# Kernel optimization log

Hardware: AMD Instinct MI355X
Metric: run time of the kernel (lower is better)

## Reference

```python
import jax, jax.numpy as jnp
import numpy as np

S = 32  # spatial_size
EPS = 1e-8

def _adaptive_avg_pool(x, s):
    b, c, h, w = x.shape
    kh, kw = h // s, w // s
    return x.reshape(b, c, s, kh, s, kw).mean(axis=(3, 5))

def _gram_cosine(x):
    # x: [B, C, s, s] -> rows: [B*s*s, C]
    b, c, s, _ = x.shape
    rows = x.reshape(b, c, s * s).transpose(0, 2, 1).reshape(b * s * s, c)
    norms = jnp.sqrt(jnp.sum(rows * rows, axis=-1, keepdims=True))
    xn = rows / jnp.maximum(norms, EPS)
    return xn @ xn.T  # [N, N]

def setup_inputs() -> dict:
    key = jax.random.key(0)
    k1, k2 = jax.random.split(key)
    p1 = jax.random.normal(k1, (8, 64, 128, 128), dtype=jnp.float32)
    p2 = jax.random.normal(k2, (8, 64, 128, 128), dtype=jnp.float32)
    return {"p1": p1, "p2": p2}

def reference(p1, p2):
    sim_a = _gram_cosine(_adaptive_avg_pool(p1, S))
    sim_b = _gram_cosine(_adaptive_avg_pool(p2, S))
    return jnp.mean((sim_a - sim_b) ** 2)
```

## Files before the change

kernel.cpp:

```cpp
#include <hip/hip_runtime.h>

typedef float f4 __attribute__((ext_vector_type(4)));
typedef float f2 __attribute__((ext_vector_type(2)));

#define PAD 68
#define NPART 256
#define PART_STRIDE 12288


__device__ __forceinline__ void lds_barrier() {
    asm volatile("s_waitcnt lgkmcnt(0)" ::: "memory");
    __builtin_amdgcn_s_barrier();
    __builtin_amdgcn_sched_barrier(0);
}

__global__ __launch_bounds__(1024) void fused_gram_kernel(
    const float* __restrict__ p1, const float* __restrict__ p2,
    float* __restrict__ partials, unsigned* __restrict__ cnt)
{
    __shared__ float la[2][8 * PAD];
    __shared__ float lb[2][8 * PAD];
    const int t  = threadIdx.x;
    const int b  = blockIdx.x >> 5;
    const int oi = blockIdx.x & 31;

    if (blockIdx.x == 0 && t == 0) *cnt = 0u;

    const int m   = t >> 9;
    const int c   = (t >> 3) & 63;
    const int oj8 = t & 7;
    const float* src = m ? p2 : p1;
    const long base = (long)((b * 64 + c) * 128 + oi * 4) * 128 + oj8 * 4;
    float* dst0 = m ? lb[0] : la[0];
    float* dst1 = m ? lb[1] : la[1];

    const int l  = t & 63;
    const int w  = t >> 6;
    const int nm = w >> 3, nr = w & 7;

    const int c1 = (t >> 5) * 2;
    const int c2 = (t & 31) * 2;
    f2 aa0 = {}, aa1 = {}, ab0 = {}, ab1 = {}, bb0 = {}, bb1 = {};

    auto issue = [&](int q, f4& R0, f4& R1, f4& R2, f4& R3) {
        const float* s = src + base + q * 32;
        R0 = *(const f4*)(s);
        R1 = *(const f4*)(s + 128);
        R2 = *(const f4*)(s + 256);
        R3 = *(const f4*)(s + 384);
    };
    auto pool = [&](const f4& R0, const f4& R1, const f4& R2, const f4& R3,
                    float* dst) {
        const f4 v = (R0 + R1) + (R2 + R3);
        dst[oj8 * PAD + c] = ((v[0] + v[1]) + (v[2] + v[3])) * 0.0625f;
    };
    auto normphase = [&](int bi) {
        float* rowp = (nm ? lb[bi] : la[bi]) + nr * PAD;
        const float v = rowp[l];
        float ss = v * v;
        ss += __shfl_xor(ss, 1);
        ss += __shfl_xor(ss, 2);
        ss += __shfl_xor(ss, 4);
        ss += __shfl_xor(ss, 8);
        ss += __shfl_xor(ss, 16);
        ss += __shfl_xor(ss, 32);
        rowp[l] = v * (1.0f / fmaxf(sqrtf(ss), 1e-8f));
    };
    auto gram = [&](int bi) {
        #pragma unroll
        for (int r = 0; r < 8; ++r) {
            const f2 a1 = *(const f2*)&la[bi][r * PAD + c1];
            const f2 a2 = *(const f2*)&la[bi][r * PAD + c2];
            const f2 b1 = *(const f2*)&lb[bi][r * PAD + c1];
            const f2 b2 = *(const f2*)&lb[bi][r * PAD + c2];
            aa0 += a2 * a1[0];  aa1 += a2 * a1[1];
            ab0 += b2 * a1[0];  ab1 += b2 * a1[1];
            bb0 += b2 * b1[0];  bb1 += b2 * b1[1];
        }
    };

    f4 A0, A1, A2, A3, B0, B1, B2, B3;
    issue(0, A0, A1, A2, A3);
    issue(1, B0, B1, B2, B3);

    pool(A0, A1, A2, A3, dst0);  lds_barrier();
    normphase(0);                lds_barrier();
    issue(2, A0, A1, A2, A3);
    gram(0);

    pool(B0, B1, B2, B3, dst1);  lds_barrier();
    normphase(1);                lds_barrier();
    issue(3, B0, B1, B2, B3);
    gram(1);

    pool(A0, A1, A2, A3, dst0);  lds_barrier();
    normphase(0);                lds_barrier();
    gram(0);

    pool(B0, B1, B2, B3, dst1);  lds_barrier();
    normphase(1);                lds_barrier();
    gram(1);

    float* P = partials + (long)blockIdx.x * PART_STRIDE;
    *(f2*)&P[0 * 4096 + (c1    ) * 64 + c2] = aa0;
    *(f2*)&P[0 * 4096 + (c1 + 1) * 64 + c2] = aa1;
    *(f2*)&P[1 * 4096 + (c1    ) * 64 + c2] = ab0;
    *(f2*)&P[1 * 4096 + (c1 + 1) * 64 + c2] = ab1;
    *(f2*)&P[2 * 4096 + (c1    ) * 64 + c2] = bb0;
    *(f2*)&P[2 * 4096 + (c1 + 1) * 64 + c2] = bb1;
}

__global__ __launch_bounds__(256) void reduce_kernel(
    const float* __restrict__ partials, float* __restrict__ bpart,
    unsigned* __restrict__ cnt, float* __restrict__ out)
{
    __shared__ float red[3][16][17];
    __shared__ float vred[16];
    __shared__ float fr[256];
    __shared__ unsigned last_flag;
    const int t  = threadIdx.x;
    const int el = t & 15;
    const int pc = t >> 4;
    const int e  = blockIdx.x * 16 + el;

    float saa = 0.f, sab = 0.f, sbb = 0.f;
    #pragma unroll 4
    for (int i = 0; i < 16; ++i) {
        const float* P = partials + (long)(pc * 16 + i) * PART_STRIDE;
        saa += P[e];
        sab += P[4096 + e];
        sbb += P[8192 + e];
    }
    red[0][el][pc] = saa; red[1][el][pc] = sab; red[2][el][pc] = sbb;
    __syncthreads();

    if (t < 16) {
        float a = 0.f, mm = 0.f, bv = 0.f;
        #pragma unroll
        for (int p = 0; p < 16; ++p) {
            a  += red[0][t][p];
            mm += red[1][t][p];
            bv += red[2][t][p];
        }
        vred[t] = fmaf(a, a, fmaf(bv, bv, -2.0f * (mm * mm)));
    }
    __syncthreads();

    if (t == 0) {
        float s = 0.f;
        #pragma unroll
        for (int i = 0; i < 16; ++i) s += vred[i];
        __hip_atomic_store(&bpart[blockIdx.x], s, __ATOMIC_RELEASE,
                           __HIP_MEMORY_SCOPE_AGENT);
        unsigned old = __hip_atomic_fetch_add(cnt, 1u, __ATOMIC_ACQ_REL,
                                              __HIP_MEMORY_SCOPE_AGENT);
        last_flag = (old == NPART - 1) ? 1u : 0u;
    }
    __syncthreads();

    if (last_flag) {
        fr[t] = __hip_atomic_load(&bpart[t], __ATOMIC_ACQUIRE,
                                  __HIP_MEMORY_SCOPE_AGENT);
        __syncthreads();
        for (int s2 = 128; s2 > 0; s2 >>= 1) {
            if (t < s2) fr[t] += fr[t + s2];
            __syncthreads();
        }
        if (t == 0) out[0] = fr[0] * (1.0f / 67108864.0f);
    }
}

extern "C" void kernel_launch(void* const* d_in, const int* in_sizes, int n_in,
                              void* d_out, int out_size, void* d_ws, size_t ws_size,
                              hipStream_t stream)
{
    const float* p1 = (const float*)d_in[0];
    const float* p2 = (const float*)d_in[1];
    float* ws       = (float*)d_ws;
    float* partials = ws;
    float* bpart    = ws + (long)NPART * PART_STRIDE;
    unsigned* cnt   = (unsigned*)(ws + 3146240);

    fused_gram_kernel<<<NPART, 1024, 0, stream>>>(p1, p2, partials, cnt);
    reduce_kernel   <<<NPART, 256, 0, stream>>>(partials, bpart, cnt, (float*)d_out);
}
```

Measured before the change: 33.67 us.

## Fuse final reduction into gram kernel via global atomics and last-block reduce

Removes the separate reduce kernel and the 256 per-block partial Gram buffers. Each block now atomically adds its 64x64x3 partial Gram values into one shared 12288-float accumulator. The last block to finish, found with an atomic counter, computes the squared-difference sum and writes the output. A memset is added to zero the accumulator and counter, and the input loads switch to nontemporal. The trade is about 12 MB of partial writes and reads plus one kernel launch against roughly 3M contended float atomics to L2 and an extra memset launch.

```diff
diff --git a/kernel.cpp b/kernel.cpp
--- a/kernel.cpp
+++ b/kernel.cpp
@@ -4,8 +4,7 @@
 typedef float f2 __attribute__((ext_vector_type(2)));
 
 #define PAD 68
-#define NPART 256
-#define PART_STRIDE 12288
+#define NBLK 256
 
 
 __device__ __forceinline__ void lds_barrier() {
@@ -14,17 +13,17 @@
     __builtin_amdgcn_sched_barrier(0);
 }
 
-__global__ __launch_bounds__(1024) void fused_gram_kernel(
+__global__ __launch_bounds__(1024) void fused_all_kernel(
     const float* __restrict__ p1, const float* __restrict__ p2,
-    float* __restrict__ partials, unsigned* __restrict__ cnt)
+    float* __restrict__ gram, unsigned* __restrict__ cnt,
+    float* __restrict__ out)
 {
     __shared__ float la[2][8 * PAD];
     __shared__ float lb[2][8 * PAD];
+    __shared__ unsigned lastf;
     const int t  = threadIdx.x;
     const int b  = blockIdx.x >> 5;
     const int oi = blockIdx.x & 31;
-
-    if (blockIdx.x == 0 && t == 0) *cnt = 0u;
 
     const int m   = t >> 9;
     const int c   = (t >> 3) & 63;
@@ -44,10 +43,10 @@
 
     auto issue = [&](int q, f4& R0, f4& R1, f4& R2, f4& R3) {
         const float* s = src + base + q * 32;
-        R0 = *(const f4*)(s);
-        R1 = *(const f4*)(s + 128);
-        R2 = *(const f4*)(s + 256);
-        R3 = *(const f4*)(s + 384);
+        R0 = __builtin_nontemporal_load((const f4*)(s));
+        R1 = __builtin_nontemporal_load((const f4*)(s + 128));
+        R2 = __builtin_nontemporal_load((const f4*)(s + 256));
+        R3 = __builtin_nontemporal_load((const f4*)(s + 384));
     };
     auto pool = [&](const f4& R0, const f4& R1, const f4& R2, const f4& R3,
                     float* dst) {
@@ -66,7 +65,7 @@
         ss += __shfl_xor(ss, 32);
         rowp[l] = v * (1.0f / fmaxf(sqrtf(ss), 1e-8f));
     };
-    auto gram = [&](int bi) {
+    auto gramacc = [&](int bi) {
         #pragma unroll
         for (int r = 0; r < 8; ++r) {
             const f2 a1 = *(const f2*)&la[bi][r * PAD + c1];
@@ -86,83 +85,58 @@
     pool(A0, A1, A2, A3, dst0);  lds_barrier();
     normphase(0);                lds_barrier();
     issue(2, A0, A1, A2, A3);
-    gram(0);
+    gramacc(0);
 
     pool(B0, B1, B2, B3, dst1);  lds_barrier();
     normphase(1);                lds_barrier();
     issue(3, B0, B1, B2, B3);
-    gram(1);
+    gramacc(1);
 
     pool(A0, A1, A2, A3, dst0);  lds_barrier();
     normphase(0);                lds_barrier();
-    gram(0);
+    gramacc(0);
 
     pool(B0, B1, B2, B3, dst1);  lds_barrier();
     normphase(1);                lds_barrier();
-    gram(1);
+    gramacc(1);
 
-    float* P = partials + (long)blockIdx.x * PART_STRIDE;
-    *(f2*)&P[0 * 4096 + (c1    ) * 64 + c2] = aa0;
-    *(f2*)&P[0 * 4096 + (c1 + 1) * 64 + c2] = aa1;
-    *(f2*)&P[1 * 4096 + (c1    ) * 64 + c2] = ab0;
-    *(f2*)&P[1 * 4096 + (c1 + 1) * 64 + c2] = ab1;
-    *(f2*)&P[2 * 4096 + (c1    ) * 64 + c2] = bb0;
-    *(f2*)&P[2 * 4096 + (c1 + 1) * 64 + c2] = bb1;
-}
+    {
+        float* G0 = gram +           c1 * 64 + c2;
+        float* G1 = gram + 4096 +    c1 * 64 + c2;
+        float* G2 = gram + 8192 +    c1 * 64 + c2;
+        atomicAdd(G0,      aa0[0]); atomicAdd(G0 + 1,  aa0[1]);
+        atomicAdd(G0 + 64, aa1[0]); atomicAdd(G0 + 65, aa1[1]);
+        atomicAdd(G1,      ab0[0]); atomicAdd(G1 + 1,  ab0[1]);
+        atomicAdd(G1 + 64, ab1[0]); atomicAdd(G1 + 65, ab1[1]);
+        atomicAdd(G2,      bb0[0]); atomicAdd(G2 + 1,  bb0[1]);
+        atomicAdd(G2 + 64, bb1[0]); atomicAdd(G2 + 65, bb1[1]);
+    }
 
-__global__ __launch_bounds__(256) void reduce_kernel(
-    const float* __restrict__ partials, float* __restrict__ bpart,
-    unsigned* __restrict__ cnt, float* __restrict__ out)
-{
-    __shared__ float red[3][16][17];
-    __shared__ float vred[16];
-    __shared__ float fr[256];
-    __shared__ unsigned last_flag;
-    const int t  = threadIdx.x;
-    const int el = t & 15;
-    const int pc = t >> 4;
-    const int e  = blockIdx.x * 16 + el;
-
-    float saa = 0.f, sab = 0.f, sbb = 0.f;
-    #pragma unroll 4
-    for (int i = 0; i < 16; ++i) {
-        const float* P = partials + (long)(pc * 16 + i) * PART_STRIDE;
-        saa += P[e];
-        sab += P[4096 + e];
-        sbb += P[8192 + e];
-    }
-    red[0][el][pc] = saa; red[1][el][pc] = sab; red[2][el][pc] = sbb;
     __syncthreads();
-
-    if (t < 16) {
-        float a = 0.f, mm = 0.f, bv = 0.f;
-        #pragma unroll
-        for (int p = 0; p < 16; ++p) {
-            a  += red[0][t][p];
-            mm += red[1][t][p];
-            bv += red[2][t][p];
-        }
-        vred[t] = fmaf(a, a, fmaf(bv, bv, -2.0f * (mm * mm)));
+    if (t == 0) {
+        unsigned old = __hip_atomic_fetch_add(cnt, 1u, __ATOMIC_ACQ_REL,
+                                              __HIP_MEMORY_SCOPE_AGENT);
+        lastf = (old == NBLK - 1) ? 1u : 0u;
     }
     __syncthreads();
 
-    if (t == 0) {
-        float s = 0.f;
+    if (lastf) {
+        float vsum = 0.f;
         #pragma unroll
-        for (int i = 0; i < 16; ++i) s += vred[i];
-        __hip_atomic_store(&bpart[blockIdx.x], s, __ATOMIC_RELEASE,
-                           __HIP_MEMORY_SCOPE_AGENT);
-        unsigned old = __hip_atomic_fetch_add(cnt, 1u, __ATOMIC_ACQ_REL,
-                                              __HIP_MEMORY_SCOPE_AGENT);
-        last_flag = (old == NPART - 1) ? 1u : 0u;
-    }
-    __syncthreads();
-
-    if (last_flag) {
-        fr[t] = __hip_atomic_load(&bpart[t], __ATOMIC_ACQUIRE,
-                                  __HIP_MEMORY_SCOPE_AGENT);
+        for (int i = 0; i < 4; ++i) {
+            const int e = t * 4 + i;
+            const float a  = __hip_atomic_load(&gram[e],
+                                __ATOMIC_RELAXED, __HIP_MEMORY_SCOPE_AGENT);
+            const float mm = __hip_atomic_load(&gram[4096 + e],
+                                __ATOMIC_RELAXED, __HIP_MEMORY_SCOPE_AGENT);
+            const float bb = __hip_atomic_load(&gram[8192 + e],
+                                __ATOMIC_RELAXED, __HIP_MEMORY_SCOPE_AGENT);
+            vsum += fmaf(a, a, fmaf(bb, bb, -2.0f * (mm * mm)));
+        }
+        float* fr = (float*)la;
+        fr[t] = vsum;
         __syncthreads();
-        for (int s2 = 128; s2 > 0; s2 >>= 1) {
+        for (int s2 = 512; s2 > 0; s2 >>= 1) {
             if (t < s2) fr[t] += fr[t + s2];
             __syncthreads();
         }
@@ -176,11 +150,11 @@
 {
     const float* p1 = (const float*)d_in[0];
     const float* p2 = (const float*)d_in[1];
-    float* ws       = (float*)d_ws;
-    float* partials = ws;
-    float* bpart    = ws + (long)NPART * PART_STRIDE;
-    unsigned* cnt   = (unsigned*)(ws + 3146240);
+    float* ws   = (float*)d_ws;
+    float* gram = ws;
+    unsigned* cnt = (unsigned*)(ws + 12288);
 
-    fused_gram_kernel<<<NPART, 1024, 0, stream>>>(p1, p2, partials, cnt);
-    reduce_kernel   <<<NPART, 256, 0, stream>>>(partials, bpart, cnt, (float*)d_out);
+    hipMemsetAsync(ws, 0, (12288 + 1) * sizeof(float), stream);
+    fused_all_kernel<<<NBLK, 1024, 0, stream>>>(p1, p2, gram, cnt,
+                                                (float*)d_out);
 }
```

Result: slower. 70.46 us (+109.3%).

## Warp-specialize gram kernel into producer/consumer waves with LDS flag sync

Applied to the files above, without the earlier changes.

Splits the 1024-thread block into 8 producer waves that load and pool the input tiles, and 8 consumer waves that normalize and accumulate the gram products. Block-wide barriers are replaced by LDS atomic counters (ready/normd/done) with spin-waits, so loading the next tile can overlap with gram computation. Consumers now compute 2x4 output tiles with f4 loads and stores instead of 2x2. The cost is spin-wait polling, each consumer thread holding twice the accumulators, and half as many threads doing each phase's arithmetic.

```diff
diff --git a/kernel.cpp b/kernel.cpp
--- a/kernel.cpp
+++ b/kernel.cpp
@@ -8,9 +8,8 @@
 #define PART_STRIDE 12288
 
 
-__device__ __forceinline__ void lds_barrier() {
+__device__ __forceinline__ void lds_fence() {
     asm volatile("s_waitcnt lgkmcnt(0)" ::: "memory");
-    __builtin_amdgcn_s_barrier();
     __builtin_amdgcn_sched_barrier(0);
 }
 
@@ -20,94 +19,131 @@
 {
     __shared__ float la[2][8 * PAD];
     __shared__ float lb[2][8 * PAD];
+    __shared__ unsigned ready[2];
+    __shared__ unsigned normd[2];
+    __shared__ unsigned done[2];
     const int t  = threadIdx.x;
     const int b  = blockIdx.x >> 5;
     const int oi = blockIdx.x & 31;
 
     if (blockIdx.x == 0 && t == 0) *cnt = 0u;
-
-    const int m   = t >> 9;
-    const int c   = (t >> 3) & 63;
-    const int oj8 = t & 7;
-    const float* src = m ? p2 : p1;
-    const long base = (long)((b * 64 + c) * 128 + oi * 4) * 128 + oj8 * 4;
-    float* dst0 = m ? lb[0] : la[0];
-    float* dst1 = m ? lb[1] : la[1];
-
-    const int l  = t & 63;
-    const int w  = t >> 6;
-    const int nm = w >> 3, nr = w & 7;
-
-    const int c1 = (t >> 5) * 2;
-    const int c2 = (t & 31) * 2;
-    f2 aa0 = {}, aa1 = {}, ab0 = {}, ab1 = {}, bb0 = {}, bb1 = {};
-
-    auto issue = [&](int q, f4& R0, f4& R1, f4& R2, f4& R3) {
-        const float* s = src + base + q * 32;
-        R0 = *(const f4*)(s);
-        R1 = *(const f4*)(s + 128);
-        R2 = *(const f4*)(s + 256);
-        R3 = *(const f4*)(s + 384);
+    if (t < 2) { ready[t] = 0u; normd[t] = 0u; done[t] = 0u; }
+    asm volatile("s_waitcnt lgkmcnt(0)" ::: "memory");
+    __builtin_amdgcn_s_barrier();
+    __builtin_amdgcn_sched_barrier(0);
+
+    const int wave = t >> 6;
+    const int lane = t & 63;
+
+    if (wave < 8) {
+        const int pt  = t;
+        const int m   = pt >> 8;
+        const int pm  = pt & 255;
+        const int cl  = pm >> 3;
+        const int oj8 = pm & 7;
+        const float* src = m ? p2 : p1;
+        const long base0 = (long)((b * 64 + cl     ) * 128 + oi * 4) * 128 + oj8 * 4;
+        const long base1 = (long)((b * 64 + cl + 32) * 128 + oi * 4) * 128 + oj8 * 4;
+        float* dst[2] = { (m ? lb[0] : la[0]), (m ? lb[1] : la[1]) };
+
+        f4 X[8], Y[8];
+        auto issue = [&](int q, f4* R) {
+            const float* s0 = src + base0 + q * 32;
+            const float* s1 = src + base1 + q * 32;
+            R[0] = *(const f4*)(s0);       R[1] = *(const f4*)(s0 + 128);
+            R[2] = *(const f4*)(s0 + 256); R[3] = *(const f4*)(s0 + 384);
+            R[4] = *(const f4*)(s1);       R[5] = *(const f4*)(s1 + 128);
+            R[6] = *(const f4*)(s1 + 256); R[7] = *(const f4*)(s1 + 384);
+        };
+        auto pool = [&](const f4* R, int buf) {
+            const f4 v0 = (R[0] + R[1]) + (R[2] + R[3]);
+            const f4 v1 = (R[4] + R[5]) + (R[6] + R[7]);
+            dst[buf][oj8 * PAD + cl]      = ((v0[0]+v0[1])+(v0[2]+v0[3])) * 0.0625f;
+            dst[buf][oj8 * PAD + cl + 32] = ((v1[0]+v1[1])+(v1[2]+v1[3])) * 0.0625f;
+        };
+        auto mark = [&](int buf) {
+            lds_fence();
+            if (lane == 0)
+                __hip_atomic_fetch_add(&ready[buf], 1u, __ATOMIC_RELAXED,
+                                       __HIP_MEMORY_SCOPE_WORKGROUP);
+        };
+        auto wait_done = [&](int buf, unsigned tgt) {
+            while (__hip_atomic_load(&done[buf], __ATOMIC_RELAXED,
+                                     __HIP_MEMORY_SCOPE_WORKGROUP) < tgt)
+                __builtin_amdgcn_s_sleep(1);
+            __builtin_amdgcn_sched_barrier(0);
+        };
+
+        issue(0, X); issue(1, Y);
+        pool(X, 0);  issue(2, X);  mark(0);
+        pool(Y, 1);  issue(3, Y);  mark(1);
+        wait_done(0, 8);  pool(X, 0);  mark(0);
+        wait_done(1, 8);  pool(Y, 1);  mark(1);
+        return;
+    }
+
+    const int ct = t - 512;
+    const int cw = ct >> 6;
+    const int c1 = (ct >> 4) * 2;
+    const int c2 = (ct & 15) * 4;
+    f4 aa[2] = {}; f4 ab[2] = {}; f4 bb[2] = {};
+
+    auto wait_flag = [&](unsigned* f, unsigned tgt) {
+        while (__hip_atomic_load(f, __ATOMIC_RELAXED,
+                                 __HIP_MEMORY_SCOPE_WORKGROUP) < tgt)
+            __builtin_amdgcn_s_sleep(1);
+        __builtin_amdgcn_sched_barrier(0);
     };
-    auto pool = [&](const f4& R0, const f4& R1, const f4& R2, const f4& R3,
-                    float* dst) {
-        const f4 v = (R0 + R1) + (R2 + R3);
-        dst[oj8 * PAD + c] = ((v[0] + v[1]) + (v[2] + v[3])) * 0.0625f;
-    };
-    auto normphase = [&](int bi) {
-        float* rowp = (nm ? lb[bi] : la[bi]) + nr * PAD;
-        const float v = rowp[l];
-        float ss = v * v;
-        ss += __shfl_xor(ss, 1);
-        ss += __shfl_xor(ss, 2);
-        ss += __shfl_xor(ss, 4);
-        ss += __shfl_xor(ss, 8);
-        ss += __shfl_xor(ss, 16);
-        ss += __shfl_xor(ss, 32);
-        rowp[l] = v * (1.0f / fmaxf(sqrtf(ss), 1e-8f));
-    };
-    auto gram = [&](int bi) {
+
+    #pragma unroll
+    for (int q = 0; q < 4; ++q) {
+        const int buf = q & 1;
+        const unsigned rp = (unsigned)(q >> 1) + 1u;
+        wait_flag(&ready[buf], 8u * rp);
+
+        {
+            float* rA = la[buf] + cw * PAD;
+            float* rB = lb[buf] + cw * PAD;
+            const float va = rA[lane], vb = rB[lane];
+            float sa = va * va, sb = vb * vb;
+            sa += __shfl_xor(sa, 1);   sb += __shfl_xor(sb, 1);
+            sa += __shfl_xor(sa, 2);   sb += __shfl_xor(sb, 2);
+            sa += __shfl_xor(sa, 4);   sb += __shfl_xor(sb, 4);
+            sa += __shfl_xor(sa, 8);   sb += __shfl_xor(sb, 8);
+            sa += __shfl_xor(sa, 16);  sb += __shfl_xor(sb, 16);
+            sa += __shfl_xor(sa, 32);  sb += __shfl_xor(sb, 32);
+            rA[lane] = va * (1.0f / fmaxf(sqrtf(sa), 1e-8f));
+            rB[lane] = vb * (1.0f / fmaxf(sqrtf(sb), 1e-8f));
+        }
+        lds_fence();
+        if (lane == 0)
+            __hip_atomic_fetch_add(&normd[buf], 1u, __ATOMIC_RELAXED,
+                                   __HIP_MEMORY_SCOPE_WORKGROUP);
+        wait_flag(&normd[buf], 8u * rp);
+
         #pragma unroll
         for (int r = 0; r < 8; ++r) {
-            const f2 a1 = *(const f2*)&la[bi][r * PAD + c1];
-            const f2 a2 = *(const f2*)&la[bi][r * PAD + c2];
-            const f2 b1 = *(const f2*)&lb[bi][r * PAD + c1];
-            const f2 b2 = *(const f2*)&lb[bi][r * PAD + c2];
-            aa0 += a2 * a1[0];  aa1 += a2 * a1[1];
-            ab0 += b2 * a1[0];  ab1 += b2 * a1[1];
-            bb0 += b2 * b1[0];  bb1 += b2 * b1[1];
-        }
-    };
-
-    f4 A0, A1, A2, A3, B0, B1, B2, B3;
-    issue(0, A0, A1, A2, A3);
-    issue(1, B0, B1, B2, B3);
-
-    pool(A0, A1, A2, A3, dst0);  lds_barrier();
-    normphase(0);                lds_barrier();
-    issue(2, A0, A1, A2, A3);
-    gram(0);
-
-    pool(B0, B1, B2, B3, dst1);  lds_barrier();
-    normphase(1);                lds_barrier();
-    issue(3, B0, B1, B2, B3);
-    gram(1);
-
-    pool(A0, A1, A2, A3, dst0);  lds_barrier();
-    normphase(0);                lds_barrier();
-    gram(0);
-
-    pool(B0, B1, B2, B3, dst1);  lds_barrier();
-    normphase(1);                lds_barrier();
-    gram(1);
+            const f2 a1 = *(const f2*)&la[buf][r * PAD + c1];
+            const f4 a2 = *(const f4*)&la[buf][r * PAD + c2];
+            const f2 b1 = *(const f2*)&lb[buf][r * PAD + c1];
+            const f4 b2 = *(const f4*)&lb[buf][r * PAD + c2];
+            aa[0] += a2 * a1[0];  aa[1] += a2 * a1[1];
+            ab[0] += b2 * a1[0];  ab[1] += b2 * a1[1];
+            bb[0] += b2 * b1[0];  bb[1] += b2 * b1[1];
+        }
+        lds_fence();
+        if (lane == 0)
+            __hip_atomic_fetch_add(&done[buf], 1u, __ATOMIC_RELAXED,
+                                   __HIP_MEMORY_SCOPE_WORKGROUP);
+    }
 
     float* P = partials + (long)blockIdx.x * PART_STRIDE;
-    *(f2*)&P[0 * 4096 + (c1    ) * 64 + c2] = aa0;
-    *(f2*)&P[0 * 4096 + (c1 + 1) * 64 + c2] = aa1;
-    *(f2*)&P[1 * 4096 + (c1    ) * 64 + c2] = ab0;
-    *(f2*)&P[1 * 4096 + (c1 + 1) * 64 + c2] = ab1;
-    *(f2*)&P[2 * 4096 + (c1    ) * 64 + c2] = bb0;
-    *(f2*)&P[2 * 4096 + (c1 + 1) * 64 + c2] = bb1;
+    #pragma unroll
+    for (int i = 0; i < 2; ++i) {
+        *(f4*)&P[0 * 4096 + (c1 + i) * 64 + c2] = aa[i];
+        *(f4*)&P[1 * 4096 + (c1 + i) * 64 + c2] = ab[i];
+        *(f4*)&P[2 * 4096 + (c1 + i) * 64 + c2] = bb[i];
+    }
 }
 
 __global__ __launch_bounds__(256) void reduce_kernel(
```

After: 74.67 us. +121.8%, slower.

## Split each gram block into two half-width blocks and overlap loads with pooling

Applied to the files above, without the earlier changes.

The gram kernel now launches 512 blocks of 512 threads. Each block covers half of an output row (4 pooled columns instead of 8) and each thread accumulates a 2x4 gram tile. The next prefetch is issued right after pooling, before the barrier, so it overlaps the normalization phase. This raises the block count across the CUs and doubles the partials buffer, so the reduce kernel sums 32 partials per thread and moves the counter offset to match.

```diff
diff --git a/kernel.cpp b/kernel.cpp
--- a/kernel.cpp
+++ b/kernel.cpp
@@ -4,8 +4,9 @@
 typedef float f2 __attribute__((ext_vector_type(2)));
 
 #define PAD 68
-#define NPART 256
+#define NPART 512
 #define PART_STRIDE 12288
+#define NBLK2 256
 
 
 __device__ __forceinline__ void lds_barrier() {
@@ -14,36 +15,39 @@
     __builtin_amdgcn_sched_barrier(0);
 }
 
-__global__ __launch_bounds__(1024) void fused_gram_kernel(
+__global__ __launch_bounds__(512) void fused_gram_kernel(
     const float* __restrict__ p1, const float* __restrict__ p2,
     float* __restrict__ partials, unsigned* __restrict__ cnt)
 {
-    __shared__ float la[2][8 * PAD];
-    __shared__ float lb[2][8 * PAD];
-    const int t  = threadIdx.x;
-    const int b  = blockIdx.x >> 5;
-    const int oi = blockIdx.x & 31;
+    __shared__ float la[2][4 * PAD];
+    __shared__ float lb[2][4 * PAD];
+    const int t   = threadIdx.x;
+    const int blk = blockIdx.x;
+    const int b   = blk >> 6;
+    const int oi  = (blk >> 1) & 31;
+    const int h   = blk & 1;
 
-    if (blockIdx.x == 0 && t == 0) *cnt = 0u;
+    if (blk == 0 && t == 0) *cnt = 0u;
 
-    const int m   = t >> 9;
-    const int c   = (t >> 3) & 63;
-    const int oj8 = t & 7;
+    const int m   = t >> 8;
+    const int c   = (t >> 2) & 63;
+    const int oj4 = t & 3;
     const float* src = m ? p2 : p1;
-    const long base = (long)((b * 64 + c) * 128 + oi * 4) * 128 + oj8 * 4;
+    const long base = (long)((b * 64 + c) * 128 + oi * 4) * 128
+                    + h * 64 + oj4 * 4;
     float* dst0 = m ? lb[0] : la[0];
     float* dst1 = m ? lb[1] : la[1];
 
     const int l  = t & 63;
     const int w  = t >> 6;
-    const int nm = w >> 3, nr = w & 7;
+    const int nm = w >> 2, nr = w & 3;
 
-    const int c1 = (t >> 5) * 2;
-    const int c2 = (t & 31) * 2;
-    f2 aa0 = {}, aa1 = {}, ab0 = {}, ab1 = {}, bb0 = {}, bb1 = {};
+    const int c1 = (t >> 4) * 2;
+    const int c2 = (t & 15) * 4;
+    f4 aa0 = {}, aa1 = {}, ab0 = {}, ab1 = {}, bb0 = {}, bb1 = {};
 
     auto issue = [&](int q, f4& R0, f4& R1, f4& R2, f4& R3) {
-        const float* s = src + base + q * 32;
+        const float* s = src + base + q * 16;
         R0 = *(const f4*)(s);
         R1 = *(const f4*)(s + 128);
         R2 = *(const f4*)(s + 256);
@@ -52,7 +56,7 @@
     auto pool = [&](const f4& R0, const f4& R1, const f4& R2, const f4& R3,
                     float* dst) {
         const f4 v = (R0 + R1) + (R2 + R3);
-        dst[oj8 * PAD + c] = ((v[0] + v[1]) + (v[2] + v[3])) * 0.0625f;
+        dst[oj4 * PAD + c] = ((v[0] + v[1]) + (v[2] + v[3])) * 0.0625f;
     };
     auto normphase = [&](int bi) {
         float* rowp = (nm ? lb[bi] : la[bi]) + nr * PAD;
@@ -68,11 +72,11 @@
     };
     auto gram = [&](int bi) {
         #pragma unroll
-        for (int r = 0; r < 8; ++r) {
+        for (int r = 0; r < 4; ++r) {
             const f2 a1 = *(const f2*)&la[bi][r * PAD + c1];
-            const f2 a2 = *(const f2*)&la[bi][r * PAD + c2];
+            const f4 a2 = *(const f4*)&la[bi][r * PAD + c2];
             const f2 b1 = *(const f2*)&lb[bi][r * PAD + c1];
-            const f2 b2 = *(const f2*)&lb[bi][r * PAD + c2];
+            const f4 b2 = *(const f4*)&lb[bi][r * PAD + c2];
             aa0 += a2 * a1[0];  aa1 += a2 * a1[1];
             ab0 += b2 * a1[0];  ab1 += b2 * a1[1];
             bb0 += b2 * b1[0];  bb1 += b2 * b1[1];
@@ -83,31 +87,25 @@
     issue(0, A0, A1, A2, A3);
     issue(1, B0, B1, B2, B3);
 
-    pool(A0, A1, A2, A3, dst0);  lds_barrier();
-    normphase(0);                lds_barrier();
-    issue(2, A0, A1, A2, A3);
-    gram(0);
+    pool(A0, A1, A2, A3, dst0);  issue(2, A0, A1, A2, A3);
+    lds_barrier();  normphase(0);  lds_barrier();  gram(0);
 
-    pool(B0, B1, B2, B3, dst1);  lds_barrier();
-    normphase(1);                lds_barrier();
-    issue(3, B0, B1, B2, B3);
-    gram(1);
+    pool(B0, B1, B2, B3, dst1);  issue(3, B0, B1, B2, B3);
+    lds_barrier();  normphase(1);  lds_barrier();  gram(1);
 
-    pool(A0, A1, A2, A3, dst0);  lds_barrier();
-    normphase(0);                lds_barrier();
-    gram(0);
+    pool(A0, A1, A2, A3, dst0);
+    lds_barrier();  normphase(0);  lds_barrier();  gram(0);
 
-    pool(B0, B1, B2, B3, dst1);  lds_barrier();
-    normphase(1);                lds_barrier();
-    gram(1);
+    pool(B0, B1, B2, B3, dst1);
+    lds_barrier();  normphase(1);  lds_barrier();  gram(1);
 
-    float* P = partials + (long)blockIdx.x * PART_STRIDE;
-    *(f2*)&P[0 * 4096 + (c1    ) * 64 + c2] = aa0;
-    *(f2*)&P[0 * 4096 + (c1 + 1) * 64 + c2] = aa1;
-    *(f2*)&P[1 * 4096 + (c1    ) * 64 + c2] = ab0;
-    *(f2*)&P[1 * 4096 + (c1 + 1) * 64 + c2] = ab1;
-    *(f2*)&P[2 * 4096 + (c1    ) * 64 + c2] = bb0;
-    *(f2*)&P[2 * 4096 + (c1 + 1) * 64 + c2] = bb1;
+    float* P = partials + (long)blk * PART_STRIDE;
+    *(f4*)&P[0 * 4096 + (c1    ) * 64 + c2] = aa0;
+    *(f4*)&P[0 * 4096 + (c1 + 1) * 64 + c2] = aa1;
+    *(f4*)&P[1 * 4096 + (c1    ) * 64 + c2] = ab0;
+    *(f4*)&P[1 * 4096 + (c1 + 1) * 64 + c2] = ab1;
+    *(f4*)&P[2 * 4096 + (c1    ) * 64 + c2] = bb0;
+    *(f4*)&P[2 * 4096 + (c1 + 1) * 64 + c2] = bb1;
 }
 
 __global__ __launch_bounds__(256) void reduce_kernel(
@@ -125,8 +123,8 @@
 
     float saa = 0.f, sab = 0.f, sbb = 0.f;
     #pragma unroll 4
-    for (int i = 0; i < 16; ++i) {
-        const float* P = partials + (long)(pc * 16 + i) * PART_STRIDE;
+    for (int i = 0; i < 32; ++i) {
+        const float* P = partials + (long)(pc * 32 + i) * PART_STRIDE;
         saa += P[e];
         sab += P[4096 + e];
         sbb += P[8192 + e];
@@ -154,7 +152,7 @@
                            __HIP_MEMORY_SCOPE_AGENT);
         unsigned old = __hip_atomic_fetch_add(cnt, 1u, __ATOMIC_ACQ_REL,
                                               __HIP_MEMORY_SCOPE_AGENT);
-        last_flag = (old == NPART - 1) ? 1u : 0u;
+        last_flag = (old == NBLK2 - 1) ? 1u : 0u;
     }
     __syncthreads();
 
@@ -179,8 +177,8 @@
     float* ws       = (float*)d_ws;
     float* partials = ws;
     float* bpart    = ws + (long)NPART * PART_STRIDE;
-    unsigned* cnt   = (unsigned*)(ws + 3146240);
+    unsigned* cnt   = (unsigned*)(ws + 6292224);
 
-    fused_gram_kernel<<<NPART, 1024, 0, stream>>>(p1, p2, partials, cnt);
-    reduce_kernel   <<<NPART, 256, 0, stream>>>(partials, bpart, cnt, (float*)d_out);
+    fused_gram_kernel<<<NPART, 512, 0, stream>>>(p1, p2, partials, cnt);
+    reduce_kernel   <<<NBLK2, 256, 0, stream>>>(partials, bpart, cnt, (float*)d_out);
 }
```

Result: slower. 40.29 us (+19.7%).
